# Optimization experiments

Hardware: AMD Instinct MI355X
Metric: run time of the kernel (lower is better)

## Reference

```python
import jax, jax.numpy as jnp
import numpy as np

N_LAYERS = 4
BATCH, IN_DIM, N_UNITS, OUT_DIM = 65536, 16, 1024, 1


def _linear(x, w, b):
    return x @ w.T + b


def setup_inputs() -> dict:
    key = jax.random.key(0)
    ks = jax.random.split(key, 18)
    s = lambda fan_in: 1.0 / np.sqrt(fan_in)
    return {
        "x": jax.random.normal(ks[0], (BATCH, IN_DIM), jnp.float32),
        "Sw_w": jax.random.normal(ks[1], (N_UNITS, IN_DIM), jnp.float32) * s(IN_DIM),
        "Sw_b": jax.random.normal(ks[2], (N_UNITS,), jnp.float32) * 0.01,
        "Uz_w": jax.random.normal(ks[3], (N_UNITS, IN_DIM), jnp.float32) * s(IN_DIM),
        "Uz_b": jax.random.normal(ks[4], (N_UNITS,), jnp.float32) * 0.01,
        "Wz_w": jax.random.normal(ks[5], (N_UNITS, N_UNITS), jnp.float32) * s(N_UNITS),
        "Wz_b": jax.random.normal(ks[6], (N_UNITS,), jnp.float32) * 0.01,
        "Ug_w": jax.random.normal(ks[7], (N_UNITS, IN_DIM), jnp.float32) * s(IN_DIM),
        "Ug_b": jax.random.normal(ks[8], (N_UNITS,), jnp.float32) * 0.01,
        "Wg_w": jax.random.normal(ks[9], (N_UNITS, N_UNITS), jnp.float32) * s(N_UNITS),
        "Wg_b": jax.random.normal(ks[10], (N_UNITS,), jnp.float32) * 0.01,
        "Ur_w": jax.random.normal(ks[11], (N_UNITS, IN_DIM), jnp.float32) * s(IN_DIM),
        "Ur_b": jax.random.normal(ks[12], (N_UNITS,), jnp.float32) * 0.01,
        "Uh_w": jax.random.normal(ks[13], (N_UNITS, IN_DIM), jnp.float32) * s(IN_DIM),
        "Uh_b": jax.random.normal(ks[14], (N_UNITS,), jnp.float32) * 0.01,
        "out_w": jax.random.normal(ks[15], (OUT_DIM, N_UNITS), jnp.float32) * s(N_UNITS),
        "out_b": jax.random.normal(ks[16], (OUT_DIM,), jnp.float32) * 0.01,
    }


def reference(x, Sw_w, Sw_b, Uz_w, Uz_b, Wz_w, Wz_b, Ug_w, Ug_b, Wg_w, Wg_b,
              Ur_w, Ur_b, Uh_w, Uh_b, out_w, out_b):
    act = jnp.tanh
    S1 = _linear(x, Sw_w, Sw_b)  # [B, H]
    # x-side projections are loop-invariant; hoist them.
    ux_z = _linear(x, Uz_w, Uz_b)
    ux_g = _linear(x, Ug_w, Ug_b)
    ux_r = _linear(x, Ur_w, Ur_b)
    ux_h = _linear(x, Uh_w, Uh_b)
    # NOTE: original forward uses Wg (not Wr/Wh) in the R and H gates — replicated faithfully.
    wgS1 = _linear(S1, Wg_w, Wg_b)  # G depends only on S1: loop-invariant
    output = None
    for i in range(N_LAYERS):
        S = S1 if i == 0 else act(output)
        Z = act(ux_z + _linear(S, Wz_w, Wz_b))
        G = act(ux_g + wgS1)
        R = act(ux_r + _linear(S, Wg_w, Wg_b))
        H = act(ux_h + _linear(S * R, Wg_w, Wg_b))
        output = (1.0 - G) * H + Z * S
    return _linear(output, out_w, out_b)
```

## Files before the change

kernel.cpp:

```cpp
#include <hip/hip_runtime.h>
#include <hip/hip_bf16.h>


typedef float f32x4 __attribute__((ext_vector_type(4)));
typedef __bf16 bf16x8 __attribute__((ext_vector_type(8)));
typedef unsigned int u32x4 __attribute__((ext_vector_type(4)));

#define MFMA16 __builtin_amdgcn_mfma_f32_16x16x32_bf16

#define WS_WZ   0u
#define WS_WG   (2u << 20)
#define WS_XT   (4u << 20)
#define WS_BIAS ((4u << 20) + 6u * 65536u)
#define WS_S    ((size_t)8 << 20)

static __device__ __forceinline__ unsigned short f2bf(float f) {
    __hip_bfloat16 h = __float2bfloat16(f);
    union { __hip_bfloat16 h; unsigned short u; } c; c.h = h; return c.u;
}
static __device__ __forceinline__ float bf2f(unsigned short u) {
    union { unsigned int u; float f; } c; c.u = ((unsigned int)u) << 16; return c.f;
}
static __device__ __forceinline__ float fast_tanh(float x) {
    float e = __expf(2.0f * x);
    return 1.0f - 2.0f * __builtin_amdgcn_rcpf(e + 1.0f);
}
static __device__ __forceinline__ unsigned int swoff(int row, int kelem) {
    unsigned int a = (unsigned int)(row * 2048 + kelem * 2);
    return a ^ (unsigned int)((row & 7) << 4);
}

__global__ void prep_big(const float* __restrict__ Wz, const float* __restrict__ Wg,
                         char* __restrict__ ws) {
    int bid = blockIdx.x;
    int mat = bid >> 11, rem = bid & 2047;
    int ks = rem >> 6, cf = rem & 63;
    const float* src = mat ? Wg : Wz;
    char* dst = ws + ((size_t)mat << 21) + ((size_t)(ks * 64 + cf) << 10);
    int l = threadIdx.x;
    int col = cf * 16 + (l & 15);
    int kb  = ks * 32 + ((l >> 4) << 3);
    unsigned short* d = (unsigned short*)(dst + l * 16);
    #pragma unroll
    for (int j = 0; j < 8; ++j) d[j] = f2bf(src[col * 1024 + kb + j]);
}

__global__ void prep_x(const float* __restrict__ Uz, const float* __restrict__ Ur,
                       const float* __restrict__ Uh, const float* __restrict__ Ug,
                       const float* __restrict__ Sw, char* __restrict__ xt) {
    int bid = blockIdx.x;
    int g_ = bid >> 6, cf = bid & 63;
    int l = threadIdx.x;
    int col = cf * 16 + (l & 15);
    int kb  = (l >> 4) << 3;
    unsigned short* d = (unsigned short*)(xt + ((size_t)(g_ * 64 + cf) << 10) + l * 16);
    #pragma unroll
    for (int j = 0; j < 8; ++j) {
        int k = kb + j;
        float v = 0.0f;
        if (k < 16) {
            int idx = col * 16 + k;
            switch (g_) {
                case 0: v = Uz[idx]; break;
                case 1: v = Ur[idx]; break;
                case 2: v = Uh[idx]; break;
                case 3: v = Ug[idx]; break;
                case 4: v = Ur[idx] - Ug[idx]; break;
                case 5: v = Sw[idx]; break;
            }
        }
        d[j] = f2bf(v);
    }
}

__global__ void prep_bias(const float* __restrict__ Uz_b, const float* __restrict__ Wz_b,
                          const float* __restrict__ Ur_b, const float* __restrict__ Uh_b,
                          const float* __restrict__ Ug_b, const float* __restrict__ Wg_b,
                          const float* __restrict__ Sw_b, float* __restrict__ dst) {
    int i = blockIdx.x * 256 + threadIdx.x;
    dst[i]        = Uz_b[i] + Wz_b[i];
    dst[1024 + i] = Ur_b[i] + Wg_b[i];
    dst[2048 + i] = Uh_b[i] + Wg_b[i];
    dst[3072 + i] = Ug_b[i] + Wg_b[i];
    dst[4096 + i] = Sw_b[i];
}


static __device__ __forceinline__ void stage_xb(const float* __restrict__ x,
                                                unsigned short* xb, int t, int tid) {
    for (int i = tid; i < 64 * 32; i += 1024) {
        int r = i >> 5, c = i & 31;
        float v = (c < 16) ? x[(size_t)(t * 64 + r) * 16 + c] : 0.0f;
        xb[i] = f2bf(v);
    }
}
static __device__ __forceinline__ void stage_S(const char* __restrict__ Sg,
                                               char* sbuf, int t, int tid) {
    for (int i = tid; i < 8192; i += 1024) {
        int r = i >> 7, c8 = i & 127;
        bf16x8 v = *(const bf16x8*)(Sg + (size_t)(t * 64 + r) * 2048 + c8 * 16);
        *(bf16x8*)(sbuf + swoff(r, c8 * 8)) = v;
    }
}
static __device__ __forceinline__ void unstage_S(const char* sbuf,
                                                 char* __restrict__ Sg, int t, int tid) {
    for (int i = tid; i < 8192; i += 1024) {
        int r = i >> 7, c8 = i & 127;
        bf16x8 v = *(const bf16x8*)(sbuf + swoff(r, c8 * 8));
        *(bf16x8*)(Sg + (size_t)(t * 64 + r) * 2048 + c8 * 16) = v;
    }
}

static __device__ __forceinline__ void mmx16(f32x4 (&acc)[4][4], const char* __restrict__ xtab,
                                             const unsigned short* xb, int lane, int wv) {
    const int c15 = lane & 15, h = lane >> 4;
    bf16x8 a[4];
    #pragma unroll
    for (int rf = 0; rf < 4; ++rf)
        a[rf] = *(const bf16x8*)(xb + (c15 + 16 * rf) * 32 + h * 8);
    #pragma unroll
    for (int cf = 0; cf < 4; ++cf) {
        bf16x8 b = *(const bf16x8*)(xtab + ((wv * 4 + cf) << 10) + lane * 16);
        #pragma unroll
        for (int rf = 0; rf < 4; ++rf) acc[rf][cf] = MFMA16(a[rf], b, acc[rf][cf], 0, 0, 0);
    }
}

static __device__ __forceinline__ void mms16(f32x4 (&acc)[4][4], const char* __restrict__ stab,
                                             const char* sb, int lane, int wv) {
    const int c15 = lane & 15, h = lane >> 4;
    #pragma unroll 2
    for (int ks = 0; ks < 32; ++ks) {
        const char* bp = stab + ((size_t)(ks * 64 + wv * 4) << 10) + lane * 16;
        bf16x8 b[4];
        #pragma unroll
        for (int cf = 0; cf < 4; ++cf) b[cf] = *(const bf16x8*)(bp + (cf << 10));
        bf16x8 a[4];
        #pragma unroll
        for (int rf = 0; rf < 4; ++rf)
            a[rf] = *(const bf16x8*)(sb + swoff(c15 + 16 * rf, (ks << 5) + (h << 3)));
        #pragma unroll
        for (int cf = 0; cf < 4; ++cf)
            #pragma unroll
            for (int rf = 0; rf < 4; ++rf)
                acc[rf][cf] = MFMA16(a[rf], b[cf], acc[rf][cf], 0, 0, 0);
    }
}

#define ZERO_ACC(acc) { _Pragma("unroll") for (int rf_ = 0; rf_ < 4; ++rf_) \
    _Pragma("unroll") for (int cf_ = 0; cf_ < 4; ++cf_) acc[rf_][cf_] = (f32x4)0.0f; }

__global__ __launch_bounds__(1024, 4)
void k_s1(const float* __restrict__ x, const char* __restrict__ ws, char* __restrict__ Sg) {
    extern __shared__ char lds[];
    char* sbuf = lds;
    unsigned short* xb = (unsigned short*)(lds + 131072);
    const int tid = threadIdx.x, lane = tid & 63, wv = tid >> 6, t = blockIdx.x;
    const int c15 = lane & 15, h = lane >> 4;
    stage_xb(x, xb, t, tid);
    __syncthreads();
    f32x4 acc[4][4];
    ZERO_ACC(acc);
    mmx16(acc, ws + WS_XT + 5 * 65536, xb, lane, wv);
    const float* BS = (const float*)(ws + WS_BIAS) + 4096;
    #pragma unroll
    for (int cf = 0; cf < 4; ++cf) {
        int col = (wv << 6) + (cf << 4) + c15;
        float b = BS[col];
        #pragma unroll
        for (int rf = 0; rf < 4; ++rf)
            #pragma unroll
            for (int r = 0; r < 4; ++r) {
                int row = (rf << 4) + (h << 2) + r;
                *(unsigned short*)(sbuf + swoff(row, col)) = f2bf(acc[rf][cf][r] + b);
            }
    }
    __syncthreads();
    unstage_S(sbuf, Sg, t, tid);
}

__global__ __launch_bounds__(1024, 4)
void k_z(const float* __restrict__ x, const char* __restrict__ ws,
         const char* __restrict__ Sg, char* __restrict__ dst, int kind) {
    extern __shared__ char lds[];
    char* sbuf = lds;
    unsigned short* xb = (unsigned short*)(lds + 131072);
    const int tid = threadIdx.x, lane = tid & 63, wv = tid >> 6, t = blockIdx.x;
    const int c15 = lane & 15, h = lane >> 4;
    stage_S(Sg, sbuf, t, tid);
    stage_xb(x, xb, t, tid);
    __syncthreads();
    f32x4 acc[4][4];
    ZERO_ACC(acc);
    mmx16(acc, ws + WS_XT + (kind ? 3 : 0) * 65536, xb, lane, wv);
    mms16(acc, ws + (kind ? WS_WG : WS_WZ), sbuf, lane, wv);
    const float* B = (const float*)(ws + WS_BIAS) + (kind ? 3072 : 0);
    unsigned int pk[32];
    #pragma unroll
    for (int cf = 0; cf < 4; ++cf) {
        int col = (wv << 6) + (cf << 4) + c15;
        float b = B[col];
        #pragma unroll
        for (int rf = 0; rf < 4; ++rf) {
            float v[4];
            #pragma unroll
            for (int r = 0; r < 4; ++r) {
                float z = fast_tanh(acc[rf][cf][r] + b);
                if (!kind) {
                    int row = (rf << 4) + (h << 2) + r;
                    z *= bf2f(*(const unsigned short*)(sbuf + swoff(row, col)));
                }
                v[r] = z;
            }
            pk[(rf * 4 + cf) * 2 + 0] = (unsigned int)f2bf(v[0]) | ((unsigned int)f2bf(v[1]) << 16);
            pk[(rf * 4 + cf) * 2 + 1] = (unsigned int)f2bf(v[2]) | ((unsigned int)f2bf(v[3]) << 16);
        }
    }
    char* dt = dst + ((size_t)t << 17);
    #pragma unroll
    for (int w = 0; w < 8; ++w) {
        u32x4 q = { pk[w * 4], pk[w * 4 + 1], pk[w * 4 + 2], pk[w * 4 + 3] };
        *(u32x4*)(dt + w * 16384 + tid * 16) = q;
    }
}

__global__ __launch_bounds__(1024, 4)
void k_rh(const float* __restrict__ x, const char* __restrict__ ws, char* __restrict__ Sg,
          const char* __restrict__ Gp, const char* __restrict__ ZSp, int last,
          const float* __restrict__ ow, const float* __restrict__ ob,
          float* __restrict__ outp) {
    extern __shared__ char lds[];
    char* sbuf = lds;
    unsigned short* xb = (unsigned short*)(lds + 131072);
    float* red = (float*)(lds + 131072 + 4096);
    const int tid = threadIdx.x, lane = tid & 63, wv = tid >> 6, t = blockIdx.x;
    const int c15 = lane & 15, h = lane >> 4;
    stage_S(Sg, sbuf, t, tid);
    stage_xb(x, xb, t, tid);
    __syncthreads();

    const float* BR = (const float*)(ws + WS_BIAS) + 1024;
    const float* BH = (const float*)(ws + WS_BIAS) + 2048;

    f32x4 acc[4][4];
    ZERO_ACC(acc);
    mmx16(acc, ws + WS_XT + 1 * 65536, xb, lane, wv);
    mms16(acc, ws + WS_WG, sbuf, lane, wv);
    unsigned int srp[32];
    #pragma unroll
    for (int cf = 0; cf < 4; ++cf) {
        int col = (wv << 6) + (cf << 4) + c15;
        float brl = BR[col];
        #pragma unroll
        for (int rf = 0; rf < 4; ++rf) {
            float v[4];
            #pragma unroll
            for (int r = 0; r < 4; ++r) {
                int row = (rf << 4) + (h << 2) + r;
                float rv = fast_tanh(acc[rf][cf][r] + brl);
                v[r] = rv * bf2f(*(const unsigned short*)(sbuf + swoff(row, col)));
            }
            srp[(rf * 4 + cf) * 2 + 0] = (unsigned int)f2bf(v[0]) | ((unsigned int)f2bf(v[1]) << 16);
            srp[(rf * 4 + cf) * 2 + 1] = (unsigned int)f2bf(v[2]) | ((unsigned int)f2bf(v[3]) << 16);
        }
    }
    __syncthreads();
    #pragma unroll
    for (int cf = 0; cf < 4; ++cf) {
        int col = (wv << 6) + (cf << 4) + c15;
        #pragma unroll
        for (int rf = 0; rf < 4; ++rf)
            #pragma unroll
            for (int r = 0; r < 4; ++r) {
                int row = (rf << 4) + (h << 2) + r;
                unsigned short u = (unsigned short)((srp[(rf * 4 + cf) * 2 + (r >> 1)] >> ((r & 1) * 16)) & 0xffff);
                *(unsigned short*)(sbuf + swoff(row, col)) = u;
            }
    }
    __syncthreads();

    ZERO_ACC(acc);
    mmx16(acc, ws + WS_XT + 2 * 65536, xb, lane, wv);
    mms16(acc, ws + WS_WG, sbuf, lane, wv);
    __syncthreads();

    const char* gt = Gp  + ((size_t)t << 17);
    const char* zt = ZSp + ((size_t)t << 17);
    if (!last) {
        #pragma unroll
        for (int w = 0; w < 8; ++w) {
            u32x4 g4 = *(const u32x4*)(gt + w * 16384 + tid * 16);
            u32x4 z4 = *(const u32x4*)(zt + w * 16384 + tid * 16);
            #pragma unroll
            for (int jj = 0; jj < 2; ++jj) {
                int rfcf = w * 2 + jj;
                int rf = rfcf >> 2, cf = rfcf & 3;
                int col = (wv << 6) + (cf << 4) + c15;
                float bhl = BH[col];
                #pragma unroll
                for (int r = 0; r < 4; ++r) {
                    int row = (rf << 4) + (h << 2) + r;
                    float g  = bf2f((unsigned short)((g4[jj * 2 + (r >> 1)] >> ((r & 1) * 16)) & 0xffff));
                    float zs = bf2f((unsigned short)((z4[jj * 2 + (r >> 1)] >> ((r & 1) * 16)) & 0xffff));
                    float hv = fast_tanh(acc[rf][cf][r] + bhl);
                    float o  = (1.0f - g) * hv + zs;
                    *(unsigned short*)(sbuf + swoff(row, col)) = f2bf(fast_tanh(o));
                }
            }
        }
        __syncthreads();
        unstage_S(sbuf, Sg, t, tid);
    } else {
        float po[16];
        #pragma unroll
        for (int i = 0; i < 16; ++i) po[i] = 0.0f;
        #pragma unroll
        for (int w = 0; w < 8; ++w) {
            u32x4 g4 = *(const u32x4*)(gt + w * 16384 + tid * 16);
            u32x4 z4 = *(const u32x4*)(zt + w * 16384 + tid * 16);
            #pragma unroll
            for (int jj = 0; jj < 2; ++jj) {
                int rfcf = w * 2 + jj;
                int rf = rfcf >> 2, cf = rfcf & 3;
                int col = (wv << 6) + (cf << 4) + c15;
                float bhl = BH[col];
                float oww = ow[col];
                #pragma unroll
                for (int r = 0; r < 4; ++r) {
                    float g  = bf2f((unsigned short)((g4[jj * 2 + (r >> 1)] >> ((r & 1) * 16)) & 0xffff));
                    float zs = bf2f((unsigned short)((z4[jj * 2 + (r >> 1)] >> ((r & 1) * 16)) & 0xffff));
                    float hv = fast_tanh(acc[rf][cf][r] + bhl);
                    po[(rf << 2) + r] += ((1.0f - g) * hv + zs) * oww;
                }
            }
        }
        #pragma unroll
        for (int off = 1; off < 16; off <<= 1)
            #pragma unroll
            for (int i = 0; i < 16; ++i) po[i] += __shfl_xor(po[i], off);
        if (c15 == 0) {
            #pragma unroll
            for (int rf = 0; rf < 4; ++rf)
                #pragma unroll
                for (int r = 0; r < 4; ++r)
                    red[wv * 64 + (rf << 4) + (h << 2) + r] = po[(rf << 2) + r];
        }
        __syncthreads();
        if (tid < 64) {
            float s = ob[0];
            #pragma unroll
            for (int w = 0; w < 16; ++w) s += red[w * 64 + tid];
            outp[t * 64 + tid] = s;
        }
    }
}


static __device__ __forceinline__ void mm_x(f32x4 acc[2][8], const char* __restrict__ xtab,
                                            const unsigned short* __restrict__ xb,
                                            int lane, int wv) {
    const int c15 = lane & 15, h = lane >> 4;
    bf16x8 a0 = *(const bf16x8*)(xb + c15 * 48 + h * 8);
    bf16x8 a1 = *(const bf16x8*)(xb + (c15 + 16) * 48 + h * 8);
    #pragma unroll
    for (int cf = 0; cf < 8; ++cf) {
        bf16x8 b = *(const bf16x8*)(xtab + ((wv * 8 + cf) << 10) + lane * 16);
        acc[0][cf] = MFMA16(a0, b, acc[0][cf], 0, 0, 0);
        acc[1][cf] = MFMA16(a1, b, acc[1][cf], 0, 0, 0);
    }
}

static __device__ __forceinline__ void mm_s(f32x4 acc[2][8], const char* __restrict__ stab,
                                            const char* __restrict__ sb, int lane, int wv) {
    const int c15 = lane & 15, h = lane >> 4;
    #pragma unroll 2
    for (int ks = 0; ks < 32; ++ks) {
        const char* bp = stab + ((size_t)(ks * 64 + wv * 8) << 10) + lane * 16;
        bf16x8 b[8];
        #pragma unroll
        for (int cf = 0; cf < 8; ++cf) b[cf] = *(const bf16x8*)(bp + (cf << 10));
        bf16x8 a0 = *(const bf16x8*)(sb + swoff(c15,      (ks << 5) + (h << 3)));
        bf16x8 a1 = *(const bf16x8*)(sb + swoff(c15 + 16, (ks << 5) + (h << 3)));
        #pragma unroll
        for (int cf = 0; cf < 8; ++cf) {
            acc[0][cf] = MFMA16(a0, b[cf], acc[0][cf], 0, 0, 0);
            acc[1][cf] = MFMA16(a1, b[cf], acc[1][cf], 0, 0, 0);
        }
    }
}

__global__ __launch_bounds__(512, 2)
void dgm_main(const float* __restrict__ x, const float* __restrict__ out_w,
              const float* __restrict__ out_b, const char* __restrict__ ws,
              float* __restrict__ out) {
    extern __shared__ char lds[];
    char* sbuf0 = lds;
    char* sbuf1 = lds + 65536;
    unsigned short* xb = (unsigned short*)(lds + 131072);
    float* red = (float*)(lds + 131072 + 3072);

    const int tid = threadIdx.x, lane = tid & 63, wv = tid >> 6;
    const int c15 = lane & 15, h = lane >> 4;
    const int t = blockIdx.x;

    const char* WZ = ws + WS_WZ;
    const char* WG = ws + WS_WG;
    const char* XT = ws + WS_XT;
    const float* BZ = (const float*)(ws + WS_BIAS);
    const float* BR = BZ + 1024;
    const float* BH = BZ + 2048;
    const float* BG = BZ + 3072;
    const float* BS = BZ + 4096;

    for (int i = tid; i < 32 * 48; i += 512) {
        int r_ = i / 48, c_ = i % 48;
        float v = (c_ < 16) ? x[(t * 32 + r_) * 16 + c_] : 0.0f;
        xb[r_ * 48 + c_] = f2bf(v);
    }
    __syncthreads();

    f32x4 acc[2][8];
    unsigned int g1m[2][8][2];
    unsigned int zs[2][8][2];
    float po[8];
    #pragma unroll
    for (int i = 0; i < 8; ++i) po[i] = 0.0f;

    #pragma unroll
    for (int rf = 0; rf < 2; ++rf)
        #pragma unroll
        for (int cf = 0; cf < 8; ++cf) acc[rf][cf] = (f32x4)0.0f;
    mm_x(acc, XT + 5 * 65536, xb, lane, wv);
    #pragma unroll
    for (int cf = 0; cf < 8; ++cf) {
        int col = (wv << 7) + (cf << 4) + c15;
        float b = BS[col];
        #pragma unroll
        for (int rf = 0; rf < 2; ++rf)
            #pragma unroll
            for (int r = 0; r < 4; ++r) {
                int row = (rf << 4) + (h << 2) + r;
                *(unsigned short*)(sbuf0 + swoff(row, col)) = f2bf(acc[rf][cf][r] + b);
            }
    }
    __syncthreads();

    {
        #pragma unroll
        for (int rf = 0; rf < 2; ++rf)
            #pragma unroll
            for (int cf = 0; cf < 8; ++cf) acc[rf][cf] = (f32x4)0.0f;
        mm_x(acc, XT + 3 * 65536, xb, lane, wv);
        mm_s(acc, WG, sbuf0, lane, wv);
        unsigned int wgx[2][8][2];
        #pragma unroll
        for (int rf = 0; rf < 2; ++rf)
            #pragma unroll
            for (int cf = 0; cf < 8; ++cf) {
                wgx[rf][cf][0] = (unsigned int)f2bf(acc[rf][cf][0]) |
                                 ((unsigned int)f2bf(acc[rf][cf][1]) << 16);
                wgx[rf][cf][1] = (unsigned int)f2bf(acc[rf][cf][2]) |
                                 ((unsigned int)f2bf(acc[rf][cf][3]) << 16);
            }
        #pragma unroll
        for (int rf = 0; rf < 2; ++rf)
            #pragma unroll
            for (int cf = 0; cf < 8; ++cf) acc[rf][cf] = (f32x4)0.0f;
        mm_x(acc, XT + 4 * 65536, xb, lane, wv);
        #pragma unroll
        for (int cf = 0; cf < 8; ++cf) {
            int col = (wv << 7) + (cf << 4) + c15;
            float brl = BR[col], bgl = BG[col];
            #pragma unroll
            for (int rf = 0; rf < 2; ++rf) {
                float g1v[4];
                #pragma unroll
                for (int r = 0; r < 4; ++r) {
                    int row = (rf << 4) + (h << 2) + r;
                    float wgv = bf2f((unsigned short)((wgx[rf][cf][r >> 1] >> ((r & 1) * 16)) & 0xffff));
                    float rv = fast_tanh(wgv + acc[rf][cf][r] + brl);
                    float s1 = bf2f(*(const unsigned short*)(sbuf0 + swoff(row, col)));
                    *(unsigned short*)(sbuf1 + swoff(row, col)) = f2bf(s1 * rv);
                    g1v[r] = 1.0f - fast_tanh(wgv + bgl);
                }
                g1m[rf][cf][0] = (unsigned int)f2bf(g1v[0]) | ((unsigned int)f2bf(g1v[1]) << 16);
                g1m[rf][cf][1] = (unsigned int)f2bf(g1v[2]) | ((unsigned int)f2bf(g1v[3]) << 16);
            }
        }
    }
    __syncthreads();

    char* cur = sbuf0;
    char* oth = sbuf1;
    #pragma clang loop unroll(disable)
    for (int L = 0; L < 4; ++L) {
        #pragma unroll
        for (int rf = 0; rf < 2; ++rf)
            #pragma unroll
            for (int cf = 0; cf < 8; ++cf) acc[rf][cf] = (f32x4)0.0f;
        mm_x(acc, XT + 0 * 65536, xb, lane, wv);
        mm_s(acc, WZ, cur, lane, wv);
        #pragma unroll
        for (int cf = 0; cf < 8; ++cf) {
            int col = (wv << 7) + (cf << 4) + c15;
            float bzl = BZ[col];
            #pragma unroll
            for (int rf = 0; rf < 2; ++rf) {
                float zv[4];
                #pragma unroll
                for (int r = 0; r < 4; ++r) {
                    int row = (rf << 4) + (h << 2) + r;
                    float z = fast_tanh(acc[rf][cf][r] + bzl);
                    float s = bf2f(*(const unsigned short*)(cur + swoff(row, col)));
                    zv[r] = z * s;
                }
                zs[rf][cf][0] = (unsigned int)f2bf(zv[0]) | ((unsigned int)f2bf(zv[1]) << 16);
                zs[rf][cf][1] = (unsigned int)f2bf(zv[2]) | ((unsigned int)f2bf(zv[3]) << 16);
            }
        }
        if (L > 0) {
            #pragma unroll
            for (int rf = 0; rf < 2; ++rf)
                #pragma unroll
                for (int cf = 0; cf < 8; ++cf) acc[rf][cf] = (f32x4)0.0f;
            mm_x(acc, XT + 1 * 65536, xb, lane, wv);
            mm_s(acc, WG, cur, lane, wv);
            #pragma unroll
            for (int cf = 0; cf < 8; ++cf) {
                int col = (wv << 7) + (cf << 4) + c15;
                float brl = BR[col];
                #pragma unroll
                for (int rf = 0; rf < 2; ++rf)
                    #pragma unroll
                    for (int r = 0; r < 4; ++r) {
                        int row = (rf << 4) + (h << 2) + r;
                        float rv = fast_tanh(acc[rf][cf][r] + brl);
                        float s = bf2f(*(const unsigned short*)(cur + swoff(row, col)));
                        *(unsigned short*)(oth + swoff(row, col)) = f2bf(s * rv);
                    }
            }
        }
        __syncthreads();
        #pragma unroll
        for (int rf = 0; rf < 2; ++rf)
            #pragma unroll
            for (int cf = 0; cf < 8; ++cf) acc[rf][cf] = (f32x4)0.0f;
        mm_x(acc, XT + 2 * 65536, xb, lane, wv);
        mm_s(acc, WG, oth, lane, wv);
        __syncthreads();
        if (L < 3) {
            #pragma unroll
            for (int cf = 0; cf < 8; ++cf) {
                int col = (wv << 7) + (cf << 4) + c15;
                float bhl = BH[col];
                #pragma unroll
                for (int rf = 0; rf < 2; ++rf)
                    #pragma unroll
                    for (int r = 0; r < 4; ++r) {
                        int row = (rf << 4) + (h << 2) + r;
                        float hv = fast_tanh(acc[rf][cf][r] + bhl);
                        float g1 = bf2f((unsigned short)((g1m[rf][cf][r >> 1] >> ((r & 1) * 16)) & 0xffff));
                        float zsv = bf2f((unsigned short)((zs[rf][cf][r >> 1] >> ((r & 1) * 16)) & 0xffff));
                        float o = g1 * hv + zsv;
                        *(unsigned short*)(oth + swoff(row, col)) = f2bf(fast_tanh(o));
                    }
            }
        } else {
            #pragma unroll
            for (int cf = 0; cf < 8; ++cf) {
                int col = (wv << 7) + (cf << 4) + c15;
                float bhl = BH[col];
                float oww = out_w[col];
                #pragma unroll
                for (int rf = 0; rf < 2; ++rf)
                    #pragma unroll
                    for (int r = 0; r < 4; ++r) {
                        float hv = fast_tanh(acc[rf][cf][r] + bhl);
                        float g1 = bf2f((unsigned short)((g1m[rf][cf][r >> 1] >> ((r & 1) * 16)) & 0xffff));
                        float zsv = bf2f((unsigned short)((zs[rf][cf][r >> 1] >> ((r & 1) * 16)) & 0xffff));
                        po[(rf << 2) + r] += (g1 * hv + zsv) * oww;
                    }
            }
        }
        __syncthreads();
        char* tmp = cur; cur = oth; oth = tmp;
    }

    #pragma unroll
    for (int off = 1; off < 16; off <<= 1)
        #pragma unroll
        for (int i = 0; i < 8; ++i) po[i] += __shfl_xor(po[i], off);
    if (c15 == 0) {
        #pragma unroll
        for (int rf = 0; rf < 2; ++rf)
            #pragma unroll
            for (int r = 0; r < 4; ++r)
                red[wv * 32 + (rf << 4) + (h << 2) + r] = po[(rf << 2) + r];
    }
    __syncthreads();
    if (tid < 32) {
        float s = out_b[0];
        #pragma unroll
        for (int w = 0; w < 8; ++w) s += red[w * 32 + tid];
        out[t * 32 + tid] = s;
    }
}

extern "C" void kernel_launch(void* const* d_in, const int* in_sizes, int n_in,
                              void* d_out, int out_size, void* d_ws, size_t ws_size,
                              hipStream_t stream) {
    (void)in_sizes; (void)n_in; (void)out_size;
    const float* x    = (const float*)d_in[0];
    const float* Sw_w = (const float*)d_in[1];
    const float* Sw_b = (const float*)d_in[2];
    const float* Uz_w = (const float*)d_in[3];
    const float* Uz_b = (const float*)d_in[4];
    const float* Wz_w = (const float*)d_in[5];
    const float* Wz_b = (const float*)d_in[6];
    const float* Ug_w = (const float*)d_in[7];
    const float* Ug_b = (const float*)d_in[8];
    const float* Wg_w = (const float*)d_in[9];
    const float* Wg_b = (const float*)d_in[10];
    const float* Ur_w = (const float*)d_in[11];
    const float* Ur_b = (const float*)d_in[12];
    const float* Uh_w = (const float*)d_in[13];
    const float* Uh_b = (const float*)d_in[14];
    const float* ow   = (const float*)d_in[15];
    const float* ob   = (const float*)d_in[16];
    char* ws = (char*)d_ws;

    prep_big<<<4096, 64, 0, stream>>>(Wz_w, Wg_w, ws);
    prep_x<<<384, 64, 0, stream>>>(Uz_w, Ur_w, Uh_w, Ug_w, Sw_w, ws + WS_XT);
    prep_bias<<<4, 256, 0, stream>>>(Uz_b, Wz_b, Ur_b, Uh_b, Ug_b, Wg_b, Sw_b,
                                     (float*)(ws + WS_BIAS));

    size_t chunk_rows = 0;
    if (ws_size > WS_S) {
        size_t avail = ws_size - WS_S;
        chunk_rows = (avail / 6144) & ~(size_t)63;
        if (chunk_rows > 65536) chunk_rows = 65536;
    }

    if (chunk_rows >= 8192) {
        const int LA = 131072 + 4096;
        const int LB = 131072 + 4096 + 4096;
        hipFuncSetAttribute(reinterpret_cast<const void*>(k_s1),
                            hipFuncAttributeMaxDynamicSharedMemorySize, LA);
        hipFuncSetAttribute(reinterpret_cast<const void*>(k_z),
                            hipFuncAttributeMaxDynamicSharedMemorySize, LA);
        hipFuncSetAttribute(reinterpret_cast<const void*>(k_rh),
                            hipFuncAttributeMaxDynamicSharedMemorySize, LB);
        char* Sg  = ws + WS_S;
        char* Gp  = Sg + chunk_rows * 2048;
        char* ZSp = Gp + chunk_rows * 2048;
        for (size_t done = 0; done < 65536; done += chunk_rows) {
            size_t rows = 65536 - done;
            if (rows > chunk_rows) rows = chunk_rows;
            int grid = (int)(rows / 64);
            const float* xc = x + done * 16;
            float* oc = (float*)d_out + done;
            k_s1<<<grid, 1024, LA, stream>>>(xc, ws, Sg);
            k_z<<<grid, 1024, LA, stream>>>(xc, ws, Sg, Gp, 1);
            for (int L = 0; L < 4; ++L) {
                k_z<<<grid, 1024, LA, stream>>>(xc, ws, Sg, ZSp, 0);
                k_rh<<<grid, 1024, LB, stream>>>(xc, ws, Sg, Gp, ZSp, (L == 3) ? 1 : 0,
                                                 ow, ob, oc);
            }
        }
    } else {
        const int ldsBytes = 131072 + 3072 + 1024;
        hipFuncSetAttribute(reinterpret_cast<const void*>(dgm_main),
                            hipFuncAttributeMaxDynamicSharedMemorySize, ldsBytes);
        dgm_main<<<65536 / 32, 512, ldsBytes, stream>>>(x, ow, ob, ws, (float*)d_out);
    }
}
```

Measured before the change: 3.746 ms.

## Fuse Z-gate into layer kernel and S1 with G computation; drop ZS buffer

Merges the separate Z-gate kernel into the per-layer R/H kernel, so Z*S stays in registers and is never written to or read back from global memory. S1 and G are now produced by a single head kernel. Global S and G traffic switches to nontemporal loads and stores, and the workspace layout shrinks so larger chunks fit. The fused kernel holds 32 more packed registers per thread, which may raise register pressure at 1024 threads per block.

```diff
diff --git a/kernel.cpp b/kernel.cpp
--- a/kernel.cpp
+++ b/kernel.cpp
@@ -12,6 +12,7 @@
 #define WS_WG   (2u << 20)
 #define WS_XT   (4u << 20)
 #define WS_BIAS ((4u << 20) + 6u * 65536u)
+#define WS_S2   ((size_t)4718592)
 #define WS_S    ((size_t)8 << 20)
 
 static __device__ __forceinline__ unsigned short f2bf(float f) {
@@ -28,6 +29,12 @@
 static __device__ __forceinline__ unsigned int swoff(int row, int kelem) {
     unsigned int a = (unsigned int)(row * 2048 + kelem * 2);
     return a ^ (unsigned int)((row & 7) << 4);
+}
+static __device__ __forceinline__ u32x4 ntl4(const void* p) {
+    return __builtin_nontemporal_load((const u32x4*)p);
+}
+static __device__ __forceinline__ void nts4(void* p, u32x4 v) {
+    __builtin_nontemporal_store(v, (u32x4*)p);
 }
 
 __global__ void prep_big(const float* __restrict__ Wz, const float* __restrict__ Wg,
@@ -98,16 +105,16 @@
                                                char* sbuf, int t, int tid) {
     for (int i = tid; i < 8192; i += 1024) {
         int r = i >> 7, c8 = i & 127;
-        bf16x8 v = *(const bf16x8*)(Sg + (size_t)(t * 64 + r) * 2048 + c8 * 16);
-        *(bf16x8*)(sbuf + swoff(r, c8 * 8)) = v;
+        u32x4 v = ntl4(Sg + (size_t)(t * 64 + r) * 2048 + c8 * 16);
+        *(u32x4*)(sbuf + swoff(r, c8 * 8)) = v;
     }
 }
 static __device__ __forceinline__ void unstage_S(const char* sbuf,
                                                  char* __restrict__ Sg, int t, int tid) {
     for (int i = tid; i < 8192; i += 1024) {
         int r = i >> 7, c8 = i & 127;
-        bf16x8 v = *(const bf16x8*)(sbuf + swoff(r, c8 * 8));
-        *(bf16x8*)(Sg + (size_t)(t * 64 + r) * 2048 + c8 * 16) = v;
+        u32x4 v = *(const u32x4*)(sbuf + swoff(r, c8 * 8));
+        nts4(Sg + (size_t)(t * 64 + r) * 2048 + c8 * 16, v);
     }
 }
 
@@ -151,7 +158,8 @@
     _Pragma("unroll") for (int cf_ = 0; cf_ < 4; ++cf_) acc[rf_][cf_] = (f32x4)0.0f; }
 
 __global__ __launch_bounds__(1024, 4)
-void k_s1(const float* __restrict__ x, const char* __restrict__ ws, char* __restrict__ Sg) {
+void k_head(const float* __restrict__ x, const char* __restrict__ ws,
+            char* __restrict__ Sg, char* __restrict__ Gp) {
     extern __shared__ char lds[];
     char* sbuf = lds;
     unsigned short* xb = (unsigned short*)(lds + 131072);
@@ -177,58 +185,37 @@
     }
     __syncthreads();
     unstage_S(sbuf, Sg, t, tid);
-}
-
-__global__ __launch_bounds__(1024, 4)
-void k_z(const float* __restrict__ x, const char* __restrict__ ws,
-         const char* __restrict__ Sg, char* __restrict__ dst, int kind) {
-    extern __shared__ char lds[];
-    char* sbuf = lds;
-    unsigned short* xb = (unsigned short*)(lds + 131072);
-    const int tid = threadIdx.x, lane = tid & 63, wv = tid >> 6, t = blockIdx.x;
-    const int c15 = lane & 15, h = lane >> 4;
-    stage_S(Sg, sbuf, t, tid);
-    stage_xb(x, xb, t, tid);
-    __syncthreads();
-    f32x4 acc[4][4];
     ZERO_ACC(acc);
-    mmx16(acc, ws + WS_XT + (kind ? 3 : 0) * 65536, xb, lane, wv);
-    mms16(acc, ws + (kind ? WS_WG : WS_WZ), sbuf, lane, wv);
-    const float* B = (const float*)(ws + WS_BIAS) + (kind ? 3072 : 0);
+    mmx16(acc, ws + WS_XT + 3 * 65536, xb, lane, wv);
+    mms16(acc, ws + WS_WG, sbuf, lane, wv);
+    const float* BG = (const float*)(ws + WS_BIAS) + 3072;
     unsigned int pk[32];
     #pragma unroll
     for (int cf = 0; cf < 4; ++cf) {
         int col = (wv << 6) + (cf << 4) + c15;
-        float b = B[col];
+        float b = BG[col];
         #pragma unroll
         for (int rf = 0; rf < 4; ++rf) {
             float v[4];
             #pragma unroll
-            for (int r = 0; r < 4; ++r) {
-                float z = fast_tanh(acc[rf][cf][r] + b);
-                if (!kind) {
-                    int row = (rf << 4) + (h << 2) + r;
-                    z *= bf2f(*(const unsigned short*)(sbuf + swoff(row, col)));
-                }
-                v[r] = z;
-            }
+            for (int r = 0; r < 4; ++r) v[r] = fast_tanh(acc[rf][cf][r] + b);
             pk[(rf * 4 + cf) * 2 + 0] = (unsigned int)f2bf(v[0]) | ((unsigned int)f2bf(v[1]) << 16);
             pk[(rf * 4 + cf) * 2 + 1] = (unsigned int)f2bf(v[2]) | ((unsigned int)f2bf(v[3]) << 16);
         }
     }
-    char* dt = dst + ((size_t)t << 17);
+    char* dt = Gp + ((size_t)t << 17);
     #pragma unroll
     for (int w = 0; w < 8; ++w) {
         u32x4 q = { pk[w * 4], pk[w * 4 + 1], pk[w * 4 + 2], pk[w * 4 + 3] };
-        *(u32x4*)(dt + w * 16384 + tid * 16) = q;
+        nts4(dt + w * 16384 + tid * 16, q);
     }
 }
 
 __global__ __launch_bounds__(1024, 4)
-void k_rh(const float* __restrict__ x, const char* __restrict__ ws, char* __restrict__ Sg,
-          const char* __restrict__ Gp, const char* __restrict__ ZSp, int last,
-          const float* __restrict__ ow, const float* __restrict__ ob,
-          float* __restrict__ outp) {
+void k_lyr(const float* __restrict__ x, const char* __restrict__ ws,
+           char* __restrict__ Sg, const char* __restrict__ Gp, int last,
+           const float* __restrict__ ow, const float* __restrict__ ob,
+           float* __restrict__ outp) {
     extern __shared__ char lds[];
     char* sbuf = lds;
     unsigned short* xb = (unsigned short*)(lds + 131072);
@@ -239,10 +226,33 @@
     stage_xb(x, xb, t, tid);
     __syncthreads();
 
-    const float* BR = (const float*)(ws + WS_BIAS) + 1024;
-    const float* BH = (const float*)(ws + WS_BIAS) + 2048;
+    const float* BZ = (const float*)(ws + WS_BIAS);
+    const float* BR = BZ + 1024;
+    const float* BH = BZ + 2048;
 
     f32x4 acc[4][4];
+    ZERO_ACC(acc);
+    mmx16(acc, ws + WS_XT + 0 * 65536, xb, lane, wv);
+    mms16(acc, ws + WS_WZ, sbuf, lane, wv);
+    unsigned int zsp[32];
+    #pragma unroll
+    for (int cf = 0; cf < 4; ++cf) {
+        int col = (wv << 6) + (cf << 4) + c15;
+        float bzl = BZ[col];
+        #pragma unroll
+        for (int rf = 0; rf < 4; ++rf) {
+            float v[4];
+            #pragma unroll
+            for (int r = 0; r < 4; ++r) {
+                int row = (rf << 4) + (h << 2) + r;
+                float z = fast_tanh(acc[rf][cf][r] + bzl);
+                v[r] = z * bf2f(*(const unsigned short*)(sbuf + swoff(row, col)));
+            }
+            zsp[(rf * 4 + cf) * 2 + 0] = (unsigned int)f2bf(v[0]) | ((unsigned int)f2bf(v[1]) << 16);
+            zsp[(rf * 4 + cf) * 2 + 1] = (unsigned int)f2bf(v[2]) | ((unsigned int)f2bf(v[3]) << 16);
+        }
+    }
+
     ZERO_ACC(acc);
     mmx16(acc, ws + WS_XT + 1 * 65536, xb, lane, wv);
     mms16(acc, ws + WS_WG, sbuf, lane, wv);
@@ -284,13 +294,11 @@
     mms16(acc, ws + WS_WG, sbuf, lane, wv);
     __syncthreads();
 
-    const char* gt = Gp  + ((size_t)t << 17);
-    const char* zt = ZSp + ((size_t)t << 17);
+    const char* gt = Gp + ((size_t)t << 17);
     if (!last) {
         #pragma unroll
         for (int w = 0; w < 8; ++w) {
-            u32x4 g4 = *(const u32x4*)(gt + w * 16384 + tid * 16);
-            u32x4 z4 = *(const u32x4*)(zt + w * 16384 + tid * 16);
+            u32x4 g4 = ntl4(gt + w * 16384 + tid * 16);
             #pragma unroll
             for (int jj = 0; jj < 2; ++jj) {
                 int rfcf = w * 2 + jj;
@@ -301,7 +309,7 @@
                 for (int r = 0; r < 4; ++r) {
                     int row = (rf << 4) + (h << 2) + r;
                     float g  = bf2f((unsigned short)((g4[jj * 2 + (r >> 1)] >> ((r & 1) * 16)) & 0xffff));
-                    float zs = bf2f((unsigned short)((z4[jj * 2 + (r >> 1)] >> ((r & 1) * 16)) & 0xffff));
+                    float zs = bf2f((unsigned short)((zsp[rfcf * 2 + (r >> 1)] >> ((r & 1) * 16)) & 0xffff));
                     float hv = fast_tanh(acc[rf][cf][r] + bhl);
                     float o  = (1.0f - g) * hv + zs;
                     *(unsigned short*)(sbuf + swoff(row, col)) = f2bf(fast_tanh(o));
@@ -316,8 +324,7 @@
         for (int i = 0; i < 16; ++i) po[i] = 0.0f;
         #pragma unroll
         for (int w = 0; w < 8; ++w) {
-            u32x4 g4 = *(const u32x4*)(gt + w * 16384 + tid * 16);
-            u32x4 z4 = *(const u32x4*)(zt + w * 16384 + tid * 16);
+            u32x4 g4 = ntl4(gt + w * 16384 + tid * 16);
             #pragma unroll
             for (int jj = 0; jj < 2; ++jj) {
                 int rfcf = w * 2 + jj;
@@ -328,7 +335,7 @@
                 #pragma unroll
                 for (int r = 0; r < 4; ++r) {
                     float g  = bf2f((unsigned short)((g4[jj * 2 + (r >> 1)] >> ((r & 1) * 16)) & 0xffff));
-                    float zs = bf2f((unsigned short)((z4[jj * 2 + (r >> 1)] >> ((r & 1) * 16)) & 0xffff));
+                    float zs = bf2f((unsigned short)((zsp[rfcf * 2 + (r >> 1)] >> ((r & 1) * 16)) & 0xffff));
                     float hv = fast_tanh(acc[rf][cf][r] + bhl);
                     po[(rf << 2) + r] += ((1.0f - g) * hv + zs) * oww;
                 }
@@ -635,37 +642,31 @@
                                      (float*)(ws + WS_BIAS));
 
     size_t chunk_rows = 0;
-    if (ws_size > WS_S) {
-        size_t avail = ws_size - WS_S;
-        chunk_rows = (avail / 6144) & ~(size_t)63;
+    if (ws_size > WS_S2) {
+        size_t avail = ws_size - WS_S2;
+        chunk_rows = (avail / 4096) & ~(size_t)63;
         if (chunk_rows > 65536) chunk_rows = 65536;
     }
 
-    if (chunk_rows >= 8192) {
+    if (chunk_rows >= 4096) {
         const int LA = 131072 + 4096;
         const int LB = 131072 + 4096 + 4096;
-        hipFuncSetAttribute(reinterpret_cast<const void*>(k_s1),
+        hipFuncSetAttribute(reinterpret_cast<const void*>(k_head),
                             hipFuncAttributeMaxDynamicSharedMemorySize, LA);
-        hipFuncSetAttribute(reinterpret_cast<const void*>(k_z),
-                            hipFuncAttributeMaxDynamicSharedMemorySize, LA);
-        hipFuncSetAttribute(reinterpret_cast<const void*>(k_rh),
+        hipFuncSetAttribute(reinterpret_cast<const void*>(k_lyr),
                             hipFuncAttributeMaxDynamicSharedMemorySize, LB);
-        char* Sg  = ws + WS_S;
-        char* Gp  = Sg + chunk_rows * 2048;
-        char* ZSp = Gp + chunk_rows * 2048;
+        char* Sg = ws + WS_S2;
+        char* Gp = Sg + chunk_rows * 2048;
         for (size_t done = 0; done < 65536; done += chunk_rows) {
             size_t rows = 65536 - done;
             if (rows > chunk_rows) rows = chunk_rows;
             int grid = (int)(rows / 64);
             const float* xc = x + done * 16;
             float* oc = (float*)d_out + done;
-            k_s1<<<grid, 1024, LA, stream>>>(xc, ws, Sg);
-            k_z<<<grid, 1024, LA, stream>>>(xc, ws, Sg, Gp, 1);
-            for (int L = 0; L < 4; ++L) {
-                k_z<<<grid, 1024, LA, stream>>>(xc, ws, Sg, ZSp, 0);
-                k_rh<<<grid, 1024, LB, stream>>>(xc, ws, Sg, Gp, ZSp, (L == 3) ? 1 : 0,
-                                                 ow, ob, oc);
-            }
+            k_head<<<grid, 1024, LA, stream>>>(xc, ws, Sg, Gp);
+            for (int L = 0; L < 4; ++L)
+                k_lyr<<<grid, 1024, LB, stream>>>(xc, ws, Sg, Gp, (L == 3) ? 1 : 0,
+                                                  ow, ob, oc);
         }
     } else {
         const int ldsBytes = 131072 + 3072 + 1024;
```

Result: slower. 5.679 ms (+51.6%).
